# Kernel tuning notes

Measured on AMD Instinct MI355X. Metric: run time of the kernel, lower is better.

Reference implementation:

```python
import jax, jax.numpy as jnp
import numpy as np

TEMPERATURE = 0.9  # DiversityLoss temperature
EPS = 1e-6


def setup_inputs() -> dict:
    key = jax.random.key(0)
    kx, ke = jax.random.split(key)
    x = jax.random.normal(kx, (8, 4096, 128), dtype=jnp.float32)
    embed = jax.random.normal(ke, (2048, 128), dtype=jnp.float32)  # [codebook_size, dim]
    return {"x": x, "embed": embed}


def reference(x, embed):
    """EuclideanCodebook.forward (ema_update=True, eval mode: no buffer updates).

    Returns (quantize, embed_ind, diversity_loss).
    """
    shape = x.shape
    xf = x.reshape(-1, shape[-1])                       # [N, d]
    x_sq = jnp.sum(xf * xf, axis=1, keepdims=True)      # [N, 1]
    e_sq = jnp.sum(embed * embed, axis=1)[None, :]      # [1, K]
    confidence = -(x_sq - 2.0 * (xf @ embed.T) + e_sq)  # [N, K]
    embed_ind_flat = jnp.argmax(confidence, axis=-1)    # [N]
    # dequantize: gather codebook rows, restore leading shape
    quantize = jnp.take(embed, embed_ind_flat, axis=0).reshape(shape)
    embed_ind = embed_ind_flat.reshape(shape[:-1])
    # diversity loss: softmax over codes per point, mean over points, entropy-style sum
    point_probs = jax.nn.softmax(confidence / TEMPERATURE, axis=1)  # [N, K]
    class_probs = jnp.mean(point_probs, axis=0)                      # [K]
    diversity_loss = jnp.sum(class_probs * jnp.log(class_probs + EPS))
    return quantize, embed_ind, diversity_loss
```

## Files before the change

### kernel.cpp

```cpp
#include <hip/hip_runtime.h>
#include <math.h>

#define D        128
#define KCODES   2048
#define NPTS     32768
#define LO_SCALE 4096.0f
#define C1       3.205988979753252f
#define C2       (C1 / LO_SCALE)
#define ESQ_SCALE 1.602994489876626f

#define A_CSLICES 2
#define A_CODES   1024
#define A_NCH     (A_CODES / 64)
#define B_CSLICES 8
#define B_NCH     8

#define SW(G, r)  (((G) & 8) | (((G) ^ (r)) & 7))

typedef _Float16 half8 __attribute__((ext_vector_type(8)));
typedef float    f32x4 __attribute__((ext_vector_type(4)));

__device__ __forceinline__ void split_row_part(const float* __restrict__ src,
                                               _Float16* __restrict__ hi_row,
                                               _Float16* __restrict__ lo_row,
                                               int part, int rkey, float* ss) {
    #pragma unroll
    for (int g = 0; g < 4; ++g) {
        const int G = part * 4 + g;
        half8 h, l;
        float s = 0.0f;
        #pragma unroll
        for (int j = 0; j < 8; ++j) {
            float v = src[g * 8 + j];
            _Float16 hh = (_Float16)v;
            h[j] = hh;
            l[j] = (_Float16)((v - (float)hh) * LO_SCALE);
            s += v * v;
        }
        *ss += s;
        const int slot = SW(G, rkey);
        *(half8*)(hi_row + slot * 8) = h;
        *(half8*)(lo_row + slot * 8) = l;
    }
}

__global__ void prep_e_kernel(const float* __restrict__ embed,
                              float* __restrict__ e_sqt,
                              _Float16* __restrict__ ehi, _Float16* __restrict__ elo,
                              float* __restrict__ cacc) {
    const int tid = threadIdx.x;
    const int row = blockIdx.x * 64 + (tid >> 2);
    const int part = tid & 3;
    float ss = 0.0f;
    split_row_part(embed + (size_t)row * D + part * 32,
                   ehi + (size_t)row * D, elo + (size_t)row * D, part, row & 7, &ss);
    ss += __shfl_xor(ss, 1, 64);
    ss += __shfl_xor(ss, 2, 64);
    if (part == 0) e_sqt[row] = ss * ESQ_SCALE;
    if (part == 1) cacc[row] = 0.0f;
}

__global__ void prep_x_kernel(const float* __restrict__ x,
                              _Float16* __restrict__ xhi, _Float16* __restrict__ xlo) {
    const int tid = threadIdx.x;
    const int row = blockIdx.x * 64 + (tid >> 2);
    const int part = tid & 3;
    float ss = 0.0f;
    split_row_part(x + (size_t)row * D + part * 32,
                   xhi + (size_t)row * D, xlo + (size_t)row * D, part, row & 7, &ss);
}

__device__ __forceinline__ void dma_rows(const _Float16* __restrict__ g_base,
                                         _Float16* lds_base, int row0, int w, int lane) {
    const char* src = (const char*)g_base + (size_t)(row0 + 16 * w) * 256 + lane * 16;
    char* dst = (char*)lds_base + 16 * w * 256;
    #pragma unroll
    for (int i = 0; i < 4; ++i) {
        __builtin_amdgcn_global_load_lds(
            (const __attribute__((address_space(1))) unsigned int*)(src + i * 1024),
            (__attribute__((address_space(3))) unsigned int*)(dst + i * 1024),
            16, 0, 0);
    }
}

__global__ __launch_bounds__(256, 2)
void sweepA_kernel(const _Float16* __restrict__ xhi_g, const _Float16* __restrict__ xlo_g,
                   const _Float16* __restrict__ ehi_g, const _Float16* __restrict__ elo_g,
                   const float* __restrict__ e_sqt_g,
                   float* __restrict__ pm, float* __restrict__ pl, int* __restrict__ pidx) {
    __shared__ _Float16 EHI[2][64 * D];
    __shared__ _Float16 ELO[2][64 * D];
    __shared__ float esq_s[A_CODES];

    const int tid  = threadIdx.x;
    const int w    = tid >> 6;
    const int lane = tid & 63;
    const int col  = lane & 15;
    const int quad = lane >> 4;
    const int c0   = blockIdx.y * A_CODES;
    const int p0w  = blockIdx.x * 128 + w * 32;

    dma_rows(ehi_g, EHI[0], c0, w, lane);
    dma_rows(elo_g, ELO[0], c0, w, lane);
    for (int i = tid; i < A_CODES; i += 256) esq_s[i] = e_sqt_g[c0 + i];

    half8 ahi[2][4], alo[2][4];
    #pragma unroll
    for (int pt = 0; pt < 2; ++pt) {
        const int pr = p0w + pt * 16 + col;
        #pragma unroll
        for (int kk = 0; kk < 4; ++kk) {
            const int slot = SW(kk * 4 + quad, col & 7);
            ahi[pt][kk] = *(const half8*)(xhi_g + (size_t)pr * D + slot * 8);
            alo[pt][kk] = *(const half8*)(xlo_g + (size_t)pr * D + slot * 8);
        }
    }

    float lrun[2][4], bv[2][4];
    int   bi[2][4];
    #pragma unroll
    for (int pt = 0; pt < 2; ++pt)
        #pragma unroll
        for (int r = 0; r < 4; ++r) { lrun[pt][r] = 0.f; bv[pt][r] = -INFINITY; bi[pt][r] = 0; }

    __syncthreads();

    for (int ch = 0; ch < A_NCH; ++ch) {
        const int cur = ch & 1;
        if (ch + 1 < A_NCH) {
            dma_rows(ehi_g, EHI[cur ^ 1], c0 + (ch + 1) * 64, w, lane);
            dma_rows(elo_g, ELO[cur ^ 1], c0 + (ch + 1) * 64, w, lane);
        }
        const _Float16* ehi = EHI[cur];
        const _Float16* elo = ELO[cur];

        #pragma unroll
        for (int ct = 0; ct < 4; ++ct) {
            f32x4 chh[2], cx[2];
            #pragma unroll
            for (int pt = 0; pt < 2; ++pt) { chh[pt] = (f32x4){0,0,0,0}; cx[pt] = (f32x4){0,0,0,0}; }
            #pragma unroll
            for (int kk = 0; kk < 4; ++kk) {
                const int boff = (ct * 16 + col) * D + SW(kk * 4 + quad, col & 7) * 8;
                half8 Bhi = *(const half8*)&ehi[boff];
                half8 Blo = *(const half8*)&elo[boff];
                #pragma unroll
                for (int pt = 0; pt < 2; ++pt) {
                    chh[pt] = __builtin_amdgcn_mfma_f32_16x16x32_f16(ahi[pt][kk], Bhi, chh[pt], 0, 0, 0);
                    cx[pt]  = __builtin_amdgcn_mfma_f32_16x16x32_f16(ahi[pt][kk], Blo, cx[pt], 0, 0, 0);
                    cx[pt]  = __builtin_amdgcn_mfma_f32_16x16x32_f16(alo[pt][kk], Bhi, cx[pt], 0, 0, 0);
                }
            }
            const int lcode = ch * 64 + ct * 16 + col;
            const float esqT = esq_s[lcode];
            const int gcode = c0 + lcode;
            #pragma unroll
            for (int pt = 0; pt < 2; ++pt) {
                #pragma unroll
                for (int r = 0; r < 4; ++r) {
                    float s2 = fmaf(chh[pt][r], C1, fmaf(cx[pt][r], C2, -esqT));
                    lrun[pt][r] += exp2f(s2);
                    if (s2 > bv[pt][r]) { bv[pt][r] = s2; bi[pt][r] = gcode; }
                }
            }
        }
        __syncthreads();
    }

    #pragma unroll
    for (int pt = 0; pt < 2; ++pt) {
        #pragma unroll
        for (int r = 0; r < 4; ++r) {
            float v = bv[pt][r]; int idx = bi[pt][r]; float l = lrun[pt][r];
            #pragma unroll
            for (int off = 8; off >= 1; off >>= 1) {
                float ov = __shfl_xor(v, off, 16);
                int   oi = __shfl_xor(idx, off, 16);
                float ol = __shfl_xor(l, off, 16);
                l += ol;
                if (ov > v || (ov == v && oi < idx)) { v = ov; idx = oi; }
            }
            if (col == 0) {
                size_t o = (size_t)blockIdx.y * NPTS + p0w + pt * 16 + quad * 4 + r;
                pm[o] = v; pl[o] = l; pidx[o] = idx;
            }
        }
    }
}

__global__ void combine_kernel(const float* __restrict__ pm, const float* __restrict__ pl,
                               const int* __restrict__ pidx,
                               float* __restrict__ r_buf, int* __restrict__ idx_buf,
                               float* __restrict__ ind_out) {
    const int p = blockIdx.x * 256 + threadIdx.x;
    float bm = -INFINITY; int bi = 0; float l = 0.0f;
    #pragma unroll
    for (int sl = 0; sl < A_CSLICES; ++sl) {
        size_t o = (size_t)sl * NPTS + p;
        float v = pm[o];
        l += pl[o];
        if (v > bm) { bm = v; bi = pidx[o]; }
    }
    r_buf[p] = 1.0f / l;
    idx_buf[p] = bi;
    ind_out[p] = (float)bi;
}

__global__ __launch_bounds__(256, 2)
void sweepB_kernel(const _Float16* __restrict__ xhi_g, const _Float16* __restrict__ xlo_g,
                   const _Float16* __restrict__ ehi_g, const _Float16* __restrict__ elo_g,
                   const float* __restrict__ e_sqt_g, const float* __restrict__ r_buf,
                   float* __restrict__ classacc) {
    __shared__ _Float16 XHI[2][64 * D];
    __shared__ _Float16 XLO[2][64 * D];
    __shared__ float rs[2][64];

    const int tid  = threadIdx.x;
    const int w    = tid >> 6;
    const int lane = tid & 63;
    const int col  = lane & 15;
    const int quad = lane >> 4;
    const int pbase0 = blockIdx.x * (64 * B_NCH);
    const int c0w  = blockIdx.y * 256 + w * 64;

    dma_rows(xhi_g, XHI[0], pbase0, w, lane);
    dma_rows(xlo_g, XLO[0], pbase0, w, lane);
    if (tid < 64) rs[0][tid] = r_buf[pbase0 + tid];

    half8 bhi[4][4], blo[4][4];
    float esq_r[4];
    #pragma unroll
    for (int ct = 0; ct < 4; ++ct) {
        const int cr = c0w + ct * 16 + col;
        esq_r[ct] = e_sqt_g[cr];
        #pragma unroll
        for (int kk = 0; kk < 4; ++kk) {
            const int slot = SW(kk * 4 + quad, col & 7);
            bhi[ct][kk] = *(const half8*)(ehi_g + (size_t)cr * D + slot * 8);
            blo[ct][kk] = *(const half8*)(elo_g + (size_t)cr * D + slot * 8);
        }
    }

    float csum[4] = {0.f, 0.f, 0.f, 0.f};
    __syncthreads();

    for (int ch = 0; ch < B_NCH; ++ch) {
        const int cur = ch & 1;
        if (ch + 1 < B_NCH) {
            dma_rows(xhi_g, XHI[cur ^ 1], pbase0 + (ch + 1) * 64, w, lane);
            dma_rows(xlo_g, XLO[cur ^ 1], pbase0 + (ch + 1) * 64, w, lane);
            if (tid < 64) rs[cur ^ 1][tid] = r_buf[pbase0 + (ch + 1) * 64 + tid];
        }
        const _Float16* xhi = XHI[cur];
        const _Float16* xlo = XLO[cur];

        #pragma unroll
        for (int p = 0; p < 4; ++p) {
            f32x4 chh[4], cx[4];
            #pragma unroll
            for (int ct = 0; ct < 4; ++ct) { chh[ct] = (f32x4){0,0,0,0}; cx[ct] = (f32x4){0,0,0,0}; }
            #pragma unroll
            for (int kk = 0; kk < 4; ++kk) {
                const int aoff = (p * 16 + col) * D + SW(kk * 4 + quad, col & 7) * 8;
                half8 Ahi = *(const half8*)&xhi[aoff];
                half8 Alo = *(const half8*)&xlo[aoff];
                #pragma unroll
                for (int ct = 0; ct < 4; ++ct) {
                    chh[ct] = __builtin_amdgcn_mfma_f32_16x16x32_f16(Ahi, bhi[ct][kk], chh[ct], 0, 0, 0);
                    cx[ct]  = __builtin_amdgcn_mfma_f32_16x16x32_f16(Ahi, blo[ct][kk], cx[ct], 0, 0, 0);
                    cx[ct]  = __builtin_amdgcn_mfma_f32_16x16x32_f16(Alo, bhi[ct][kk], cx[ct], 0, 0, 0);
                }
            }
            const f32x4 rr = *(const f32x4*)&rs[cur][p * 16 + quad * 4];
            #pragma unroll
            for (int ct = 0; ct < 4; ++ct) {
                #pragma unroll
                for (int r = 0; r < 4; ++r) {
                    float s2 = fmaf(chh[ct][r], C1, fmaf(cx[ct][r], C2, -esq_r[ct]));
                    csum[ct] += exp2f(s2) * rr[r];
                }
            }
        }
        __syncthreads();
    }

    #pragma unroll
    for (int ct = 0; ct < 4; ++ct) {
        float v = csum[ct];
        v += __shfl_xor(v, 16, 64);
        v += __shfl_xor(v, 32, 64);
        if (quad == 0) atomicAdd(&classacc[c0w + ct * 16 + col], v);
    }
}

__global__ void gather_kernel(const float* __restrict__ embed,
                              const int* __restrict__ idx_buf,
                              float* __restrict__ q_out) {
    const int j = blockIdx.x * 256 + threadIdx.x;
    const int row = j >> 5;
    const int d4 = j & 31;
    reinterpret_cast<float4*>(q_out)[(size_t)row * 32 + d4] =
        reinterpret_cast<const float4*>(embed)[(size_t)idx_buf[row] * 32 + d4];
}

__global__ void finalize_kernel(const float* __restrict__ classacc,
                                float* __restrict__ loss_out, int N, int K) {
    __shared__ float red[256];
    const int tid = threadIdx.x;
    float s = 0.0f;
    const float invN = 1.0f / (float)N;
    for (int i = tid; i < K; i += 256) {
        float cp = classacc[i] * invN;
        s += cp * logf(cp + 1e-6f);
    }
    red[tid] = s;
    __syncthreads();
    for (int off = 128; off > 0; off >>= 1) {
        if (tid < off) red[tid] += red[tid + off];
        __syncthreads();
    }
    if (tid == 0) loss_out[0] = red[0];
}

extern "C" void kernel_launch(void* const* d_in, const int* in_sizes, int n_in,
                              void* d_out, int out_size, void* d_ws, size_t ws_size,
                              hipStream_t stream) {
    const float* x     = (const float*)d_in[0];
    const float* embed = (const float*)d_in[1];

    float* out      = (float*)d_out;
    float* q_out    = out;
    float* ind_out  = out + (size_t)NPTS * D;
    float* loss_out = ind_out + NPTS;

    float*    e_sqt = (float*)d_ws;
    float*    cacc  = e_sqt + KCODES;
    _Float16* ehi   = (_Float16*)(cacc + KCODES);
    _Float16* elo   = ehi + (size_t)KCODES * D;
    _Float16* xhi   = elo + (size_t)KCODES * D;
    _Float16* xlo   = xhi + (size_t)NPTS * D;
    float*    pm    = (float*)(xlo + (size_t)NPTS * D);
    float*    pl    = pm + (size_t)A_CSLICES * NPTS;
    int*      pidx  = (int*)(pl + (size_t)A_CSLICES * NPTS);
    float*    r_buf = (float*)(pidx + (size_t)A_CSLICES * NPTS);
    int*      idx_buf = (int*)(r_buf + NPTS);

    prep_e_kernel<<<KCODES / 64, 256, 0, stream>>>(embed, e_sqt, ehi, elo, cacc);
    prep_x_kernel<<<NPTS / 64, 256, 0, stream>>>(x, xhi, xlo);
    sweepA_kernel<<<dim3(NPTS / 128, A_CSLICES), 256, 0, stream>>>(
        xhi, xlo, ehi, elo, e_sqt, pm, pl, pidx);
    combine_kernel<<<NPTS / 256, 256, 0, stream>>>(pm, pl, pidx, r_buf, idx_buf, ind_out);
    sweepB_kernel<<<dim3(NPTS / 512, B_CSLICES), 256, 0, stream>>>(
        xhi, xlo, ehi, elo, e_sqt, r_buf, cacc);
    gather_kernel<<<NPTS * 32 / 256, 256, 0, stream>>>(embed, idx_buf, q_out);
    finalize_kernel<<<1, 256, 0, stream>>>(cacc, loss_out, NPTS, KCODES);
}
```

Baseline: 203.1 us.

## Restructure sweeps into smaller code tiles, more slices, shared-memory bins, fused prep

```diff
diff --git a/kernel.cpp b/kernel.cpp
--- a/kernel.cpp
+++ b/kernel.cpp
@@ -9,13 +9,11 @@
 #define C2       (C1 / LO_SCALE)
 #define ESQ_SCALE 1.602994489876626f
 
-#define A_CSLICES 2
-#define A_CODES   1024
-#define A_NCH     (A_CODES / 64)
-#define B_CSLICES 8
-#define B_NCH     8
-
-#define SW(G, r)  (((G) & 8) | (((G) ^ (r)) & 7))
+#define A_CSLICES 4
+#define A_CODES   512
+#define A_NCH     (A_CODES / 32)
+
+#define SW(G, r)  (((G) ^ (r)) & 15)
 
 typedef _Float16 half8 __attribute__((ext_vector_type(8)));
 typedef float    f32x4 __attribute__((ext_vector_type(4)));
@@ -44,38 +42,36 @@
     }
 }
 
-__global__ void prep_e_kernel(const float* __restrict__ embed,
-                              float* __restrict__ e_sqt,
-                              _Float16* __restrict__ ehi, _Float16* __restrict__ elo,
-                              float* __restrict__ cacc) {
+__global__ void prep_kernel(const float* __restrict__ embed, const float* __restrict__ x,
+                            float* __restrict__ e_sqt,
+                            _Float16* __restrict__ ehi, _Float16* __restrict__ elo,
+                            _Float16* __restrict__ xhi, _Float16* __restrict__ xlo,
+                            float* __restrict__ cacc) {
+    const int b = blockIdx.x;
     const int tid = threadIdx.x;
-    const int row = blockIdx.x * 64 + (tid >> 2);
     const int part = tid & 3;
     float ss = 0.0f;
-    split_row_part(embed + (size_t)row * D + part * 32,
-                   ehi + (size_t)row * D, elo + (size_t)row * D, part, row & 7, &ss);
-    ss += __shfl_xor(ss, 1, 64);
-    ss += __shfl_xor(ss, 2, 64);
-    if (part == 0) e_sqt[row] = ss * ESQ_SCALE;
-    if (part == 1) cacc[row] = 0.0f;
-}
-
-__global__ void prep_x_kernel(const float* __restrict__ x,
-                              _Float16* __restrict__ xhi, _Float16* __restrict__ xlo) {
-    const int tid = threadIdx.x;
-    const int row = blockIdx.x * 64 + (tid >> 2);
-    const int part = tid & 3;
-    float ss = 0.0f;
-    split_row_part(x + (size_t)row * D + part * 32,
-                   xhi + (size_t)row * D, xlo + (size_t)row * D, part, row & 7, &ss);
-}
-
-__device__ __forceinline__ void dma_rows(const _Float16* __restrict__ g_base,
-                                         _Float16* lds_base, int row0, int w, int lane) {
-    const char* src = (const char*)g_base + (size_t)(row0 + 16 * w) * 256 + lane * 16;
-    char* dst = (char*)lds_base + 16 * w * 256;
-    #pragma unroll
-    for (int i = 0; i < 4; ++i) {
+    if (b < KCODES / 64) {
+        const int row = b * 64 + (tid >> 2);
+        split_row_part(embed + (size_t)row * D + part * 32,
+                       ehi + (size_t)row * D, elo + (size_t)row * D, part, row & 15, &ss);
+        ss += __shfl_xor(ss, 1, 64);
+        ss += __shfl_xor(ss, 2, 64);
+        if (part == 0) e_sqt[row] = ss * ESQ_SCALE;
+        if (part == 1) cacc[row] = 0.0f;
+    } else {
+        const int row = (b - KCODES / 64) * 64 + (tid >> 2);
+        split_row_part(x + (size_t)row * D + part * 32,
+                       xhi + (size_t)row * D, xlo + (size_t)row * D, part, row & 15, &ss);
+    }
+}
+
+__device__ __forceinline__ void dma32(const _Float16* __restrict__ g_base,
+                                      _Float16* lds_base, int row0, int w, int lane) {
+    const char* src = (const char*)g_base + (size_t)(row0 + 8 * w) * 256 + lane * 16;
+    char* dst = (char*)lds_base + 8 * w * 256;
+    #pragma unroll
+    for (int i = 0; i < 2; ++i) {
         __builtin_amdgcn_global_load_lds(
             (const __attribute__((address_space(1))) unsigned int*)(src + i * 1024),
             (__attribute__((address_space(3))) unsigned int*)(dst + i * 1024),
@@ -83,13 +79,29 @@
     }
 }
 
-__global__ __launch_bounds__(256, 2)
+__device__ __forceinline__ void load_a(const _Float16* __restrict__ xhi_g,
+                                       const _Float16* __restrict__ xlo_g,
+                                       int p0w, int col, int quad,
+                                       half8 ahi[2][4], half8 alo[2][4]) {
+    #pragma unroll
+    for (int pt = 0; pt < 2; ++pt) {
+        const int pr = p0w + pt * 16 + col;
+        #pragma unroll
+        for (int kk = 0; kk < 4; ++kk) {
+            const int slot = SW(kk * 4 + quad, col);
+            ahi[pt][kk] = *(const half8*)(xhi_g + (size_t)pr * D + slot * 8);
+            alo[pt][kk] = *(const half8*)(xlo_g + (size_t)pr * D + slot * 8);
+        }
+    }
+}
+
+__global__ __launch_bounds__(256, 4)
 void sweepA_kernel(const _Float16* __restrict__ xhi_g, const _Float16* __restrict__ xlo_g,
                    const _Float16* __restrict__ ehi_g, const _Float16* __restrict__ elo_g,
                    const float* __restrict__ e_sqt_g,
                    float* __restrict__ pm, float* __restrict__ pl, int* __restrict__ pidx) {
-    __shared__ _Float16 EHI[2][64 * D];
-    __shared__ _Float16 ELO[2][64 * D];
+    __shared__ _Float16 EHI[2][32 * D];
+    __shared__ _Float16 ELO[2][32 * D];
     __shared__ float esq_s[A_CODES];
 
     const int tid  = threadIdx.x;
@@ -100,21 +112,12 @@
     const int c0   = blockIdx.y * A_CODES;
     const int p0w  = blockIdx.x * 128 + w * 32;
 
-    dma_rows(ehi_g, EHI[0], c0, w, lane);
-    dma_rows(elo_g, ELO[0], c0, w, lane);
+    dma32(ehi_g, EHI[0], c0, w, lane);
+    dma32(elo_g, ELO[0], c0, w, lane);
     for (int i = tid; i < A_CODES; i += 256) esq_s[i] = e_sqt_g[c0 + i];
 
     half8 ahi[2][4], alo[2][4];
-    #pragma unroll
-    for (int pt = 0; pt < 2; ++pt) {
-        const int pr = p0w + pt * 16 + col;
-        #pragma unroll
-        for (int kk = 0; kk < 4; ++kk) {
-            const int slot = SW(kk * 4 + quad, col & 7);
-            ahi[pt][kk] = *(const half8*)(xhi_g + (size_t)pr * D + slot * 8);
-            alo[pt][kk] = *(const half8*)(xlo_g + (size_t)pr * D + slot * 8);
-        }
-    }
+    load_a(xhi_g, xlo_g, p0w, col, quad, ahi, alo);
 
     float lrun[2][4], bv[2][4];
     int   bi[2][4];
@@ -128,22 +131,22 @@
     for (int ch = 0; ch < A_NCH; ++ch) {
         const int cur = ch & 1;
         if (ch + 1 < A_NCH) {
-            dma_rows(ehi_g, EHI[cur ^ 1], c0 + (ch + 1) * 64, w, lane);
-            dma_rows(elo_g, ELO[cur ^ 1], c0 + (ch + 1) * 64, w, lane);
-        }
-        const _Float16* ehi = EHI[cur];
-        const _Float16* elo = ELO[cur];
-
-        #pragma unroll
-        for (int ct = 0; ct < 4; ++ct) {
+            dma32(ehi_g, EHI[cur ^ 1], c0 + (ch + 1) * 32, w, lane);
+            dma32(elo_g, ELO[cur ^ 1], c0 + (ch + 1) * 32, w, lane);
+        }
+        const _Float16* eh = EHI[cur];
+        const _Float16* el = ELO[cur];
+
+        #pragma unroll
+        for (int ct = 0; ct < 2; ++ct) {
             f32x4 chh[2], cx[2];
             #pragma unroll
             for (int pt = 0; pt < 2; ++pt) { chh[pt] = (f32x4){0,0,0,0}; cx[pt] = (f32x4){0,0,0,0}; }
             #pragma unroll
             for (int kk = 0; kk < 4; ++kk) {
-                const int boff = (ct * 16 + col) * D + SW(kk * 4 + quad, col & 7) * 8;
-                half8 Bhi = *(const half8*)&ehi[boff];
-                half8 Blo = *(const half8*)&elo[boff];
+                const int boff = (ct * 16 + col) * D + SW(kk * 4 + quad, col) * 8;
+                half8 Bhi = *(const half8*)&eh[boff];
+                half8 Blo = *(const half8*)&el[boff];
                 #pragma unroll
                 for (int pt = 0; pt < 2; ++pt) {
                     chh[pt] = __builtin_amdgcn_mfma_f32_16x16x32_f16(ahi[pt][kk], Bhi, chh[pt], 0, 0, 0);
@@ -151,7 +154,7 @@
                     cx[pt]  = __builtin_amdgcn_mfma_f32_16x16x32_f16(alo[pt][kk], Bhi, cx[pt], 0, 0, 0);
                 }
             }
-            const int lcode = ch * 64 + ct * 16 + col;
+            const int lcode = ch * 32 + ct * 16 + col;
             const float esqT = esq_s[lcode];
             const int gcode = c0 + lcode;
             #pragma unroll
@@ -206,91 +209,86 @@
     ind_out[p] = (float)bi;
 }
 
-__global__ __launch_bounds__(256, 2)
+__global__ __launch_bounds__(256, 4)
 void sweepB_kernel(const _Float16* __restrict__ xhi_g, const _Float16* __restrict__ xlo_g,
                    const _Float16* __restrict__ ehi_g, const _Float16* __restrict__ elo_g,
                    const float* __restrict__ e_sqt_g, const float* __restrict__ r_buf,
                    float* __restrict__ classacc) {
-    __shared__ _Float16 XHI[2][64 * D];
-    __shared__ _Float16 XLO[2][64 * D];
-    __shared__ float rs[2][64];
+    __shared__ _Float16 EHI[2][32 * D];
+    __shared__ _Float16 ELO[2][32 * D];
+    __shared__ float esq_s[A_CODES];
+    __shared__ float bins[A_CODES];
 
     const int tid  = threadIdx.x;
     const int w    = tid >> 6;
     const int lane = tid & 63;
     const int col  = lane & 15;
     const int quad = lane >> 4;
-    const int pbase0 = blockIdx.x * (64 * B_NCH);
-    const int c0w  = blockIdx.y * 256 + w * 64;
-
-    dma_rows(xhi_g, XHI[0], pbase0, w, lane);
-    dma_rows(xlo_g, XLO[0], pbase0, w, lane);
-    if (tid < 64) rs[0][tid] = r_buf[pbase0 + tid];
-
-    half8 bhi[4][4], blo[4][4];
-    float esq_r[4];
-    #pragma unroll
-    for (int ct = 0; ct < 4; ++ct) {
-        const int cr = c0w + ct * 16 + col;
-        esq_r[ct] = e_sqt_g[cr];
-        #pragma unroll
-        for (int kk = 0; kk < 4; ++kk) {
-            const int slot = SW(kk * 4 + quad, col & 7);
-            bhi[ct][kk] = *(const half8*)(ehi_g + (size_t)cr * D + slot * 8);
-            blo[ct][kk] = *(const half8*)(elo_g + (size_t)cr * D + slot * 8);
-        }
-    }
-
-    float csum[4] = {0.f, 0.f, 0.f, 0.f};
+    const int c0   = blockIdx.y * A_CODES;
+    const int p0w  = blockIdx.x * 128 + w * 32;
+
+    dma32(ehi_g, EHI[0], c0, w, lane);
+    dma32(elo_g, ELO[0], c0, w, lane);
+    for (int i = tid; i < A_CODES; i += 256) { esq_s[i] = e_sqt_g[c0 + i]; bins[i] = 0.0f; }
+
+    half8 ahi[2][4], alo[2][4];
+    load_a(xhi_g, xlo_g, p0w, col, quad, ahi, alo);
+
+    float rr[2][4];
+    #pragma unroll
+    for (int pt = 0; pt < 2; ++pt)
+        #pragma unroll
+        for (int r = 0; r < 4; ++r)
+            rr[pt][r] = r_buf[p0w + pt * 16 + quad * 4 + r];
+
     __syncthreads();
 
-    for (int ch = 0; ch < B_NCH; ++ch) {
+    for (int ch = 0; ch < A_NCH; ++ch) {
         const int cur = ch & 1;
-        if (ch + 1 < B_NCH) {
-            dma_rows(xhi_g, XHI[cur ^ 1], pbase0 + (ch + 1) * 64, w, lane);
-            dma_rows(xlo_g, XLO[cur ^ 1], pbase0 + (ch + 1) * 64, w, lane);
-            if (tid < 64) rs[cur ^ 1][tid] = r_buf[pbase0 + (ch + 1) * 64 + tid];
-        }
-        const _Float16* xhi = XHI[cur];
-        const _Float16* xlo = XLO[cur];
-
-        #pragma unroll
-        for (int p = 0; p < 4; ++p) {
-            f32x4 chh[4], cx[4];
-            #pragma unroll
-            for (int ct = 0; ct < 4; ++ct) { chh[ct] = (f32x4){0,0,0,0}; cx[ct] = (f32x4){0,0,0,0}; }
+        if (ch + 1 < A_NCH) {
+            dma32(ehi_g, EHI[cur ^ 1], c0 + (ch + 1) * 32, w, lane);
+            dma32(elo_g, ELO[cur ^ 1], c0 + (ch + 1) * 32, w, lane);
+        }
+        const _Float16* eh = EHI[cur];
+        const _Float16* el = ELO[cur];
+
+        #pragma unroll
+        for (int ct = 0; ct < 2; ++ct) {
+            f32x4 chh[2], cx[2];
+            #pragma unroll
+            for (int pt = 0; pt < 2; ++pt) { chh[pt] = (f32x4){0,0,0,0}; cx[pt] = (f32x4){0,0,0,0}; }
             #pragma unroll
             for (int kk = 0; kk < 4; ++kk) {
-                const int aoff = (p * 16 + col) * D + SW(kk * 4 + quad, col & 7) * 8;
-                half8 Ahi = *(const half8*)&xhi[aoff];
-                half8 Alo = *(const half8*)&xlo[aoff];
+                const int boff = (ct * 16 + col) * D + SW(kk * 4 + quad, col) * 8;
+                half8 Bhi = *(const half8*)&eh[boff];
+                half8 Blo = *(const half8*)&el[boff];
                 #pragma unroll
-                for (int ct = 0; ct < 4; ++ct) {
-                    chh[ct] = __builtin_amdgcn_mfma_f32_16x16x32_f16(Ahi, bhi[ct][kk], chh[ct], 0, 0, 0);
-                    cx[ct]  = __builtin_amdgcn_mfma_f32_16x16x32_f16(Ahi, blo[ct][kk], cx[ct], 0, 0, 0);
-                    cx[ct]  = __builtin_amdgcn_mfma_f32_16x16x32_f16(Alo, bhi[ct][kk], cx[ct], 0, 0, 0);
+                for (int pt = 0; pt < 2; ++pt) {
+                    chh[pt] = __builtin_amdgcn_mfma_f32_16x16x32_f16(ahi[pt][kk], Bhi, chh[pt], 0, 0, 0);
+                    cx[pt]  = __builtin_amdgcn_mfma_f32_16x16x32_f16(ahi[pt][kk], Blo, cx[pt], 0, 0, 0);
+                    cx[pt]  = __builtin_amdgcn_mfma_f32_16x16x32_f16(alo[pt][kk], Bhi, cx[pt], 0, 0, 0);
                 }
             }
-            const f32x4 rr = *(const f32x4*)&rs[cur][p * 16 + quad * 4];
-            #pragma unroll
-            for (int ct = 0; ct < 4; ++ct) {
+            const int lcode = ch * 32 + ct * 16 + col;
+            const float esqT = esq_s[lcode];
+            float wsum = 0.0f;
+            #pragma unroll
+            for (int pt = 0; pt < 2; ++pt) {
                 #pragma unroll
                 for (int r = 0; r < 4; ++r) {
-                    float s2 = fmaf(chh[ct][r], C1, fmaf(cx[ct][r], C2, -esq_r[ct]));
-                    csum[ct] += exp2f(s2) * rr[r];
+                    float s2 = fmaf(chh[pt][r], C1, fmaf(cx[pt][r], C2, -esqT));
+                    wsum += exp2f(s2) * rr[pt][r];
                 }
             }
+            wsum += __shfl_xor(wsum, 16, 64);
+            wsum += __shfl_xor(wsum, 32, 64);
+            if (quad == 0) atomicAdd(&bins[lcode], wsum);
         }
         __syncthreads();
     }
 
-    #pragma unroll
-    for (int ct = 0; ct < 4; ++ct) {
-        float v = csum[ct];
-        v += __shfl_xor(v, 16, 64);
-        v += __shfl_xor(v, 32, 64);
-        if (quad == 0) atomicAdd(&classacc[c0w + ct * 16 + col], v);
-    }
+    for (int i = tid; i < A_CODES; i += 256)
+        atomicAdd(&classacc[c0 + i], bins[i]);
 }
 
 __global__ void gather_kernel(const float* __restrict__ embed,
@@ -345,12 +343,12 @@
     float*    r_buf = (float*)(pidx + (size_t)A_CSLICES * NPTS);
     int*      idx_buf = (int*)(r_buf + NPTS);
 
-    prep_e_kernel<<<KCODES / 64, 256, 0, stream>>>(embed, e_sqt, ehi, elo, cacc);
-    prep_x_kernel<<<NPTS / 64, 256, 0, stream>>>(x, xhi, xlo);
+    prep_kernel<<<KCODES / 64 + NPTS / 64, 256, 0, stream>>>(
+        embed, x, e_sqt, ehi, elo, xhi, xlo, cacc);
     sweepA_kernel<<<dim3(NPTS / 128, A_CSLICES), 256, 0, stream>>>(
         xhi, xlo, ehi, elo, e_sqt, pm, pl, pidx);
     combine_kernel<<<NPTS / 256, 256, 0, stream>>>(pm, pl, pidx, r_buf, idx_buf, ind_out);
-    sweepB_kernel<<<dim3(NPTS / 512, B_CSLICES), 256, 0, stream>>>(
+    sweepB_kernel<<<dim3(NPTS / 128, A_CSLICES), 256, 0, stream>>>(
         xhi, xlo, ehi, elo, e_sqt, r_buf, cacc);
     gather_kernel<<<NPTS * 32 / 256, 256, 0, stream>>>(embed, idx_buf, q_out);
     finalize_kernel<<<1, 256, 0, stream>>>(cacc, loss_out, NPTS, KCODES);
```

Measured after the change: 229.6 us. 13.1% more time.
